# Kernel optimization log

Measured on AMD Instinct MI355X. Metric: run time of the kernel, lower is better.

## Reference

```python
import jax, jax.numpy as jnp
import numpy as np

BS, NA, NL, NF = 1024, 64, 32, 16   # batch, agents, num_link, num_link_fea
H, M, A = 32, 32, 16                # hidden_dim, message_dim, action_dim


def setup_inputs() -> dict:
    key = jax.random.key(0)
    ks = iter(jax.random.split(key, 64))
    def rn(shape, s=0.05):
        return jax.random.normal(next(ks), shape, jnp.float32) * s
    return {
        "states": jax.random.normal(next(ks), (BS, NA, NL, NF), jnp.float32),
        "hidden_state": jax.random.normal(next(ks), (BS, NA, H), jnp.float32),
        # input_attention (embed=32, heads=4)
        "ia_wq": rn((NF, H)), "ia_bq": jnp.zeros((H,), jnp.float32),
        "ia_wkv": rn((NF, 2 * H)), "ia_bkv": jnp.zeros((2 * H,), jnp.float32),
        "ia_wo": rn((H, NF)), "ia_bo": jnp.zeros((NF,), jnp.float32),
        "ln1_g": jnp.ones((NF,), jnp.float32), "ln1_b": jnp.zeros((NF,), jnp.float32),
        "il_w": rn((NL * NF, H)), "il_b": jnp.zeros((H,), jnp.float32),
        # GRUCell (gate order: r, z, n)
        "gru_wih": rn((H, 3 * H)), "gru_whh": rn((H, 3 * H)),
        "gru_bih": jnp.zeros((3 * H,), jnp.float32), "gru_bhh": jnp.zeros((3 * H,), jnp.float32),
        "ms_w": rn((H, H)), "ms_b": jnp.zeros((H,), jnp.float32),
        # per-agent message generators stacked [NA, H, M]
        "mg_w": rn((NA, H, M)), "mg_b": jnp.zeros((NA, M), jnp.float32),
        # attention_message (embed=32, heads=2)
        "ma_wq": rn((H, H)), "ma_bq": jnp.zeros((H,), jnp.float32),
        "ma_wkv": rn((M, 2 * H)), "ma_bkv": jnp.zeros((2 * H,), jnp.float32),
        "ma_wo": rn((H, H)), "ma_bo": jnp.zeros((H,), jnp.float32),
        "ln2_g": jnp.ones((H,), jnp.float32), "ln2_b": jnp.zeros((H,), jnp.float32),
        "qs_w": rn((H + M, H)), "qs_b": jnp.zeros((H,), jnp.float32),
        # per-agent Q heads stacked [NA, H, A]
        "ah_w": rn((NA, H, A)), "ah_b": jnp.zeros((NA, A), jnp.float32),
    }


def _ln(x, g, b, eps=1e-5):
    m = x.mean(-1, keepdims=True)
    v = ((x - m) ** 2).mean(-1, keepdims=True)
    return (x - m) * jax.lax.rsqrt(v + eps) * g + b


def _mha(q, kv, wq, bq, wkv, bkv, wo, bo, nh):
    # q, kv: [bs, na, sl, fd]
    bs, na, sl, _ = q.shape
    Q = q @ wq + bq
    K, V = jnp.split(kv @ wkv + bkv, 2, axis=-1)
    E = Q.shape[-1]
    hd = E // nh
    def sp(x):
        return x.reshape(bs, na, sl, nh, hd).transpose(0, 1, 3, 2, 4)  # [b,a,n,s,d]
    Qh, Kh, Vh = sp(Q), sp(K), sp(V)
    attn = jax.nn.softmax(
        jnp.einsum('banqd,bankd->banqk', Qh, Kh) * (1.0 / np.sqrt(hd)), axis=-1)
    o = jnp.einsum('banqk,bankd->banqd', attn, Vh)
    o = o.transpose(0, 1, 3, 2, 4).reshape(bs, na, sl, E)
    return o @ wo + bo


def reference(states, hidden_state,
              ia_wq, ia_bq, ia_wkv, ia_bkv, ia_wo, ia_bo,
              ln1_g, ln1_b, il_w, il_b,
              gru_wih, gru_whh, gru_bih, gru_bhh,
              ms_w, ms_b, mg_w, mg_b,
              ma_wq, ma_bq, ma_wkv, ma_bkv, ma_wo, ma_bo,
              ln2_g, ln2_b, qs_w, qs_b, ah_w, ah_b):
    bs, na, nl, nf = states.shape
    # self-attention over links + residual layernorm
    aft = _mha(states, states, ia_wq, ia_bq, ia_wkv, ia_bkv, ia_wo, ia_bo, 4)
    aft = _ln(states + aft, ln1_g, ln1_b)
    enc = aft.reshape(bs, na, nl * nf) @ il_w + il_b          # [bs, na, H]
    hprev = hidden_state.reshape(bs, na, -1)
    # GRUCell step (pytorch gate order r, z, n)
    gi = enc @ gru_wih + gru_bih
    gh = hprev @ gru_whh + gru_bhh
    ir, iz, ig = jnp.split(gi, 3, axis=-1)
    hr, hz, hg = jnp.split(gh, 3, axis=-1)
    r = jax.nn.sigmoid(ir + hr)
    z = jax.nn.sigmoid(iz + hz)
    n = jnp.tanh(ig + r * hg)
    h = (1.0 - z) * n + z * hprev                             # [bs, na, H]
    # per-agent messages
    memb = jax.nn.relu(h @ ms_w + ms_b)
    messages = jnp.einsum('bah,ahm->bam', memb, mg_w) + mg_b  # [bs, na, M]
    md = jax.lax.stop_gradient(messages)
    mean_message = (md.sum(1, keepdims=True) - md + messages) / na
    # communication attention (sl = 1) + residual layernorm
    after = _mha(h[:, :, None, :], mean_message[:, :, None, :],
                 ma_wq, ma_bq, ma_wkv, ma_bkv, ma_wo, ma_bo, 2)[:, :, 0, :]
    after = _ln(h + after, ln2_g, ln2_b)
    feat = jnp.concatenate([h, after], axis=-1)
    qemb = jax.nn.relu(feat @ qs_w + qs_b)
    q_values = jnp.einsum('bah,ahk->bak', qemb, ah_w) + ah_b  # [bs, na, A]
    return q_values, h, mean_message
```

## Files before the change

### kernel.cpp

```cpp
#include <hip/hip_runtime.h>

typedef unsigned int u32;
typedef _Float16 f16;
typedef f16 h2 __attribute__((ext_vector_type(2)));

#define QP     0
#define KVP    256
#define WOP    768
#define ILWP   1024
#define WIHP   9216
#define WHHP   11264
#define MSWP   13312
#define MGWP   13824
#define QSWP   46592
#define AHWP   47616
#define F32B   64000
#define BQ     (F32B+0)
#define BKV    (F32B+32)
#define BO     (F32B+96)
#define LN1G   (F32B+112)
#define LN1B   (F32B+128)
#define ILB    (F32B+144)
#define BIH    (F32B+176)
#define BHH    (F32B+272)
#define MSB    (F32B+368)
#define MGB    (F32B+400)
#define MAWKVV (F32B+2448)
#define MABKVV (F32B+3472)
#define MAWO   (F32B+3504)
#define MABO   (F32B+4528)
#define LN2G   (F32B+4560)
#define LN2B   (F32B+4592)
#define QSB    (F32B+4624)
#define AHB    (F32B+4656)
#define W_TOTAL (F32B+5680)
#define W_ALLOC 69696

#define OUT_Q  0
#define OUT_H  1048576
#define OUT_MM 3145728

#define CS (0.35355339059327373f * 1.4426950408889634f)

#if __has_builtin(__builtin_amdgcn_wave_barrier)
#define WB() __builtin_amdgcn_wave_barrier()
#else
#define WB() __threadfence_block()
#endif

#if __has_builtin(__builtin_amdgcn_exp2f)
__device__ __forceinline__ float EXP2(float x) { return __builtin_amdgcn_exp2f(x); }
#else
__device__ __forceinline__ float EXP2(float x) { return __expf(x * 0.6931471805599453f); }
#endif

#if __has_builtin(__builtin_amdgcn_fdot2)
__device__ __forceinline__ float FD(h2 a, h2 b, float c) {
    return __builtin_amdgcn_fdot2(a, b, c, false);
}
#else
__device__ __forceinline__ float FD(h2 a, h2 b, float c) {
    return c + (float)a.x * (float)b.x + (float)a.y * (float)b.y;
}
#endif

#if __has_builtin(__builtin_amdgcn_cvt_pkrtz)
__device__ __forceinline__ h2 pk2(float a, float b) {
    auto r = __builtin_amdgcn_cvt_pkrtz(a, b);
    h2 out;
    __builtin_memcpy(&out, &r, sizeof(out));
    return out;
}
#else
__device__ __forceinline__ h2 pk2(float a, float b) { h2 r; r.x = (f16)a; r.y = (f16)b; return r; }
#endif

__device__ __forceinline__ h2  u2h(u32 x) { union { u32 u; h2 h; } c; c.u = x; return c.h; }
__device__ __forceinline__ u32 h2u(h2 x)  { union { u32 u; h2 h; } c; c.h = x; return c.u; }

__device__ __forceinline__ float sigm(float x) { return 1.0f / (1.0f + __expf(-x)); }

struct WP { const float* p[30]; };

__global__ void kw_conv(WP wp, float* W) {
    u32* Wu = (u32*)W;
    int gid = blockIdx.x * blockDim.x + threadIdx.x;
    if (gid >= W_TOTAL) return;
    if (gid < KVP) {
        int e = gid >> 3, i = gid & 7;
        const float* wq = wp.p[0];
        Wu[gid] = h2u(pk2(wq[(2*i)*32 + e] * CS, wq[(2*i+1)*32 + e] * CS));
    } else if (gid < WOP) {
        int idx = gid - KVP; int e = idx >> 3, i = idx & 7;
        const float* wkv = wp.p[2];
        Wu[gid] = h2u(pk2(wkv[(2*i)*64 + e], wkv[(2*i+1)*64 + e]));
    } else if (gid < ILWP) {
        int idx = gid - WOP; int f = idx >> 4, i = idx & 15;
        const float* wo = wp.p[4];
        Wu[gid] = h2u(pk2(wo[(2*i)*16 + f], wo[(2*i+1)*16 + f]));
    } else if (gid < WIHP) {
        int idx = gid - ILWP;
        int jp4 = idx >> 7, t = (idx >> 2) & 31, i = idx & 3;
        int jp = jp4 * 4 + i;
        const float* ilw = wp.p[8];
        Wu[gid] = h2u(pk2(ilw[(2*jp)*32 + t], ilw[(2*jp+1)*32 + t]));
    } else if (gid < WHHP) {
        int idx = gid - WIHP;
        int kp = idx >> 7, t = (idx >> 2) & 31, j = idx & 3;
        const float* wih = wp.p[10];
        Wu[gid] = (j < 3) ? h2u(pk2(wih[(2*kp)*96 + j*32 + t], wih[(2*kp+1)*96 + j*32 + t])) : 0u;
    } else if (gid < MSWP) {
        int idx = gid - WHHP;
        int kp = idx >> 7, t = (idx >> 2) & 31, j = idx & 3;
        const float* whh = wp.p[11];
        Wu[gid] = (j < 3) ? h2u(pk2(whh[(2*kp)*96 + j*32 + t], whh[(2*kp+1)*96 + j*32 + t])) : 0u;
    } else if (gid < MGWP) {
        int idx = gid - MSWP; int kp = idx >> 5, t = idx & 31;
        const float* msw = wp.p[14];
        Wu[gid] = h2u(pk2(msw[(2*kp)*32 + t], msw[(2*kp+1)*32 + t]));
    } else if (gid < QSWP) {
        int idx = gid - MGWP; int a = idx >> 9, rem = idx & 511, kp = rem >> 5, m = rem & 31;
        const float* mgw = wp.p[16];
        Wu[gid] = h2u(pk2(mgw[(a*32 + 2*kp)*32 + m], mgw[(a*32 + 2*kp+1)*32 + m]));
    } else if (gid < AHWP) {
        int idx = gid - QSWP; int kp = idx >> 5, t = idx & 31;
        const float* qsw = wp.p[26];
        Wu[gid] = h2u(pk2(qsw[(2*kp)*32 + t], qsw[(2*kp+1)*32 + t]));
    } else if (gid < F32B) {
        int idx = gid - AHWP; int a = idx >> 8, rem = idx & 255, kp = rem >> 4, u = rem & 15;
        const float* ahw = wp.p[28];
        Wu[gid] = h2u(pk2(ahw[(a*32 + 2*kp)*16 + u], ahw[(a*32 + 2*kp+1)*16 + u]));
    } else {
        int i = gid - F32B;
        float v;
        if      (i < 32)   v = wp.p[1][i] * CS;
        else if (i < 96)   v = wp.p[3][i - 32];
        else if (i < 112)  v = wp.p[5][i - 96];
        else if (i < 128)  v = wp.p[6][i - 112];
        else if (i < 144)  v = wp.p[7][i - 128];
        else if (i < 176)  v = wp.p[9][i - 144];
        else if (i < 272)  v = wp.p[12][i - 176];
        else if (i < 368)  v = wp.p[13][i - 272];
        else if (i < 400)  v = wp.p[15][i - 368];
        else if (i < 2448) v = wp.p[17][i - 400];
        else if (i < 3472) { int j = i - 2448; v = wp.p[20][(j >> 5)*64 + 32 + (j & 31)]; }
        else if (i < 3504) v = wp.p[21][32 + (i - 3472)];
        else if (i < 4528) v = wp.p[22][i - 3504];
        else if (i < 4560) v = wp.p[23][i - 4528];
        else if (i < 4592) v = wp.p[24][i - 4560];
        else if (i < 4624) v = wp.p[25][i - 4592];
        else if (i < 4656) v = wp.p[27][i - 4624];
        else               v = wp.p[29][i - 4656];
        W[gid] = v;
    }
}

__global__ __launch_bounds__(256, 5) void k_main(
    const float* __restrict__ states, const float* __restrict__ hidden,
    const float* W, float* __restrict__ outp)
{
    const u32* Wu = (const u32*)W;

    __shared__ uint4 KbH[8][32][4];
    __shared__ uint4 VbH[8][32][4];

    const int w    = threadIdx.x >> 6;
    const int lane = threadIdx.x & 63;
    const int sub  = lane >> 5;
    const int t    = lane & 31;
    const int ag   = w * 2 + sub;
    const int pair = blockIdx.x * 4 + w;
    const int b    = pair >> 5;
    const int a    = ((pair & 31) << 1) | sub;
    const int ba   = b * 64 + a;

    float* scr = (float*)&VbH[ag][0][0];

    float s[16];
    {
        const float4* p4 = reinterpret_cast<const float4*>(states + ((size_t)ba * 32 + t) * 16);
        float4 f0 = p4[0], f1 = p4[1], f2 = p4[2], f3 = p4[3];
        s[0]=f0.x; s[1]=f0.y; s[2]=f0.z; s[3]=f0.w;
        s[4]=f1.x; s[5]=f1.y; s[6]=f1.z; s[7]=f1.w;
        s[8]=f2.x; s[9]=f2.y; s[10]=f2.z; s[11]=f2.w;
        s[12]=f3.x; s[13]=f3.y; s[14]=f3.z; s[15]=f3.w;
    }
    float hp = hidden[(size_t)ba * 32 + t];
    h2 sh[8];
    #pragma unroll
    for (int i = 0; i < 8; ++i) sh[i] = pk2(s[2*i], s[2*i+1]);

    h2 qh[16];
    #pragma unroll
    for (int j = 0; j < 16; ++j) {
        float a0 = W[BQ + 2*j], a1 = W[BQ + 2*j + 1];
        #pragma unroll
        for (int i = 0; i < 8; ++i) {
            a0 = FD(sh[i], u2h(Wu[QP + (2*j)*8 + i]), a0);
            a1 = FD(sh[i], u2h(Wu[QP + (2*j+1)*8 + i]), a1);
        }
        qh[j] = pk2(a0, a1);
    }
    #pragma unroll
    for (int u = 0; u < 4; ++u) {
        u32 kc[4], vc[4];
        #pragma unroll
        for (int c = 0; c < 4; ++c) {
            int e0 = u*8 + 2*c, e1 = e0 + 1;
            float k0 = W[BKV+e0], k1 = W[BKV+e1];
            float v0 = W[BKV+32+e0], v1 = W[BKV+32+e1];
            #pragma unroll
            for (int i = 0; i < 8; ++i) {
                k0 = FD(sh[i], u2h(Wu[KVP + e0*8 + i]), k0);
                k1 = FD(sh[i], u2h(Wu[KVP + e1*8 + i]), k1);
                v0 = FD(sh[i], u2h(Wu[KVP + (32+e0)*8 + i]), v0);
                v1 = FD(sh[i], u2h(Wu[KVP + (32+e1)*8 + i]), v1);
            }
            kc[c] = h2u(pk2(k0, k1)); vc[c] = h2u(pk2(v0, v1));
        }
        int uc = u ^ (t & 3);
        KbH[ag][t][uc] = make_uint4(kc[0], kc[1], kc[2], kc[3]);
        VbH[ag][t][uc] = make_uint4(vc[0], vc[1], vc[2], vc[3]);
    }
    WB();

    h2 oh[16];
    #pragma unroll
    for (int hh = 0; hh < 4; ++hh) {
        float l = 0.0f;
        h2 ov0 = {(f16)0, (f16)0}, ov1 = ov0, ov2 = ov0, ov3 = ov0;
        #pragma unroll
        for (int k = 0; k < 32; ++k) {
            uint4 kr = KbH[ag][k][hh ^ (k & 3)];
            float sc = 0.0f;
            sc = FD(qh[hh*4+0], u2h(kr.x), sc);
            sc = FD(qh[hh*4+1], u2h(kr.y), sc);
            sc = FD(qh[hh*4+2], u2h(kr.z), sc);
            sc = FD(qh[hh*4+3], u2h(kr.w), sc);
            float e = EXP2(sc);
            l += e;
            h2 ph = pk2(e, e);
            uint4 vr = VbH[ag][k][hh ^ (k & 3)];
            ov0 += ph * u2h(vr.x);
            ov1 += ph * u2h(vr.y);
            ov2 += ph * u2h(vr.z);
            ov3 += ph * u2h(vr.w);
        }
        float inv = 1.0f / l;
        h2 hinv = pk2(inv, inv);
        oh[hh*4+0] = ov0 * hinv; oh[hh*4+1] = ov1 * hinv;
        oh[hh*4+2] = ov2 * hinv; oh[hh*4+3] = ov3 * hinv;
    }
    WB();

    float aft[16];
    {
        float x[16];
        float mean = 0.0f;
        #pragma unroll
        for (int f = 0; f < 16; ++f) {
            float acc = W[BO + f];
            #pragma unroll
            for (int i = 0; i < 16; ++i) acc = FD(oh[i], u2h(Wu[WOP + f*16 + i]), acc);
            x[f] = s[f] + acc;
            mean += x[f];
        }
        mean *= (1.0f / 16.0f);
        float var = 0.0f;
        #pragma unroll
        for (int f = 0; f < 16; ++f) { float d = x[f] - mean; var += d * d; }
        var *= (1.0f / 16.0f);
        float rs = rsqrtf(var + 1e-5f);
        #pragma unroll
        for (int f = 0; f < 16; ++f)
            aft[f] = (x[f] - mean) * rs * W[LN1G + f] + W[LN1B + f];
    }
    uint4* aftA = &KbH[ag][0][0];
    {
        u32 ac[8];
        #pragma unroll
        for (int c = 0; c < 8; ++c) ac[c] = h2u(pk2(aft[2*c], aft[2*c+1]));
        aftA[2*t]     = make_uint4(ac[0], ac[1], ac[2], ac[3]);
        aftA[2*t + 1] = make_uint4(ac[4], ac[5], ac[6], ac[7]);
    }
    WB();

    float enc = W[ILB + t];
    {
        const uint4* aA   = aftA;
        const uint4* ilw4 = (const uint4*)(Wu + ILWP);
        #pragma unroll 8
        for (int jp4 = 0; jp4 < 64; ++jp4) {
            uint4 av = aA[jp4];
            uint4 wv = ilw4[jp4 * 32 + t];
            enc = FD(u2h(av.x), u2h(wv.x), enc);
            enc = FD(u2h(av.y), u2h(wv.y), enc);
            enc = FD(u2h(av.z), u2h(wv.z), enc);
            enc = FD(u2h(av.w), u2h(wv.w), enc);
        }
    }
    WB();
    scr[t] = enc;
    WB();

    float gi0 = W[BIH + t], gi1 = W[BIH + 32 + t], gi2 = W[BIH + 64 + t];
    float gh0 = W[BHH + t], gh1 = W[BHH + 32 + t], gh2 = W[BHH + 64 + t];
    {
        const float4* eF = (const float4*)scr;
        const float4* hF = (const float4*)(hidden + (size_t)ba * 32);
        const uint4* wi4 = (const uint4*)(Wu + WIHP);
        const uint4* wh4 = (const uint4*)(Wu + WHHP);
        #pragma unroll
        for (int q4 = 0; q4 < 8; ++q4) {
            float4 ev = eF[q4], hv = hF[q4];
            h2 ea = pk2(ev.x, ev.y), eb = pk2(ev.z, ev.w);
            h2 ha = pk2(hv.x, hv.y), hb = pk2(hv.z, hv.w);
            uint4 wiA = wi4[(q4*2)*32 + t], wiB = wi4[(q4*2+1)*32 + t];
            uint4 whA = wh4[(q4*2)*32 + t], whB = wh4[(q4*2+1)*32 + t];
            gi0 = FD(ea, u2h(wiA.x), gi0); gi1 = FD(ea, u2h(wiA.y), gi1); gi2 = FD(ea, u2h(wiA.z), gi2);
            gi0 = FD(eb, u2h(wiB.x), gi0); gi1 = FD(eb, u2h(wiB.y), gi1); gi2 = FD(eb, u2h(wiB.z), gi2);
            gh0 = FD(ha, u2h(whA.x), gh0); gh1 = FD(ha, u2h(whA.y), gh1); gh2 = FD(ha, u2h(whA.z), gh2);
            gh0 = FD(hb, u2h(whB.x), gh0); gh1 = FD(hb, u2h(whB.y), gh1); gh2 = FD(hb, u2h(whB.z), gh2);
        }
    }
    float r  = sigm(gi0 + gh0);
    float z  = sigm(gi1 + gh1);
    float n  = tanhf(gi2 + r * gh2);
    float hn = (1.0f - z) * n + z * hp;
    outp[OUT_H + (size_t)ba * 32 + t] = hn;
    WB();
    scr[64 + t] = hn;
    WB();

    {
        const float4* nF = (const float4*)(scr + 64);
        float mb = W[MSB + t];
        #pragma unroll
        for (int q4 = 0; q4 < 8; ++q4) {
            float4 v = nF[q4];
            h2 a2 = pk2(v.x, v.y), b2 = pk2(v.z, v.w);
            mb = FD(a2, u2h(Wu[MSWP + (q4*2)*32 + t]), mb);
            mb = FD(b2, u2h(Wu[MSWP + (q4*2+1)*32 + t]), mb);
        }
        mb = fmaxf(mb, 0.0f);
        WB();
        scr[96 + t] = mb;
        WB();
    }
    {
        const float4* mF = (const float4*)(scr + 96);
        float mg = W[MGB + a * 32 + t];
        #pragma unroll
        for (int q4 = 0; q4 < 8; ++q4) {
            float4 v = mF[q4];
            h2 a2 = pk2(v.x, v.y), b2 = pk2(v.z, v.w);
            mg = FD(a2, u2h(Wu[MGWP + a*512 + (q4*2)*32 + t]), mg);
            mg = FD(b2, u2h(Wu[MGWP + a*512 + (q4*2+1)*32 + t]), mg);
        }
        outp[OUT_MM + (size_t)ba * 32 + t] = mg;
    }
}

__global__ __launch_bounds__(512) void k_mean(const float* W, float* __restrict__ ao_ws,
                                              float* __restrict__ outp)
{
    const int b   = blockIdx.x;
    const int tid = threadIdx.x;
    const int t   = tid & 31;
    const int c   = tid >> 5;
    __shared__ float pS[16][32];
    __shared__ float mmS[32];

    float acc = 0.0f;
    #pragma unroll
    for (int a2 = 0; a2 < 4; ++a2)
        acc += outp[OUT_MM + ((size_t)b * 64 + (a2 * 16 + c)) * 32 + t];
    pS[c][t] = acc;
    __syncthreads();
    if (tid < 32) {
        float ssum = 0.0f;
        #pragma unroll
        for (int cc = 0; cc < 16; ++cc) ssum += pS[cc][t];
        mmS[t] = ssum * (1.0f / 64.0f);
    }
    __syncthreads();
    {
        float mv = mmS[t];
        #pragma unroll
        for (int i = 0; i < 4; ++i)
            outp[OUT_MM + (size_t)b * 2048 + i * 512 + tid] = mv;
    }
    if (tid < 32) {
        float v = W[MABKVV + t];
        #pragma unroll 8
        for (int k = 0; k < 32; ++k) v += mmS[k] * W[MAWKVV + k * 32 + t];
        float o = W[MABO + t];
        #pragma unroll 8
        for (int k = 0; k < 32; ++k) o += __shfl(v, k, 64) * W[MAWO + k * 32 + t];
        ao_ws[b * 32 + t] = o;
    }
}

__global__ __launch_bounds__(512) void k_tail(
    const float* __restrict__ ao_ws, const float* W, float* __restrict__ outp)
{
    const u32* Wu = (const u32*)W;
    __shared__ __align__(16) float featS[16][64];
    __shared__ __align__(16) float qeS[16][32];
    const int w    = threadIdx.x >> 6;
    const int lane = threadIdx.x & 63;
    const int sub  = lane >> 5;
    const int t    = lane & 31;
    const int ag   = w * 2 + sub;
    const int pair = blockIdx.x * 8 + w;
    const int b    = pair >> 5;
    const int a    = ((pair & 31) << 1) | sub;
    const int ba   = b * 64 + a;

    float h  = outp[OUT_H + (size_t)ba * 32 + t];
    float ao = ao_ws[b * 32 + t];
    float x  = h + ao;
    float sm = x;
    #pragma unroll
    for (int m2 = 1; m2 < 32; m2 <<= 1) sm += __shfl_xor(sm, m2, 64);
    float mean = sm * (1.0f / 32.0f);
    float dx = x - mean;
    float vv = dx * dx;
    #pragma unroll
    for (int m2 = 1; m2 < 32; m2 <<= 1) vv += __shfl_xor(vv, m2, 64);
    float var   = vv * (1.0f / 32.0f);
    float after = dx * rsqrtf(var + 1e-5f) * W[LN2G + t] + W[LN2B + t];

    featS[ag][t]      = h;
    featS[ag][32 + t] = after;
    WB();
    {
        const float4* fF = (const float4*)&featS[ag][0];
        float acc = W[QSB + t];
        #pragma unroll
        for (int q4 = 0; q4 < 16; ++q4) {
            float4 v = fF[q4];
            h2 a2 = pk2(v.x, v.y), b2 = pk2(v.z, v.w);
            acc = FD(a2, u2h(Wu[QSWP + (q4*2)*32 + t]), acc);
            acc = FD(b2, u2h(Wu[QSWP + (q4*2+1)*32 + t]), acc);
        }
        acc = fmaxf(acc, 0.0f);
        WB();
        qeS[ag][t] = acc;
        WB();
    }
    if (t < 16) {
        const float4* qF = (const float4*)&qeS[ag][0];
        float qa = W[AHB + a * 16 + t];
        #pragma unroll
        for (int q4 = 0; q4 < 8; ++q4) {
            float4 v = qF[q4];
            h2 a2 = pk2(v.x, v.y), b2 = pk2(v.z, v.w);
            qa = FD(a2, u2h(Wu[AHWP + a*256 + (q4*2)*16 + t]), qa);
            qa = FD(b2, u2h(Wu[AHWP + a*256 + (q4*2+1)*16 + t]), qa);
        }
        outp[OUT_Q + (size_t)ba * 16 + t] = qa;
    }
}

extern "C" void kernel_launch(void* const* d_in, const int* in_sizes, int n_in,
                              void* d_out, int out_size, void* d_ws, size_t ws_size,
                              hipStream_t stream) {
    (void)in_sizes; (void)n_in; (void)out_size; (void)ws_size;
    WP wp;
    for (int i = 0; i < 30; ++i) wp.p[i] = (const float*)d_in[i + 2];

    float* W     = (float*)d_ws;
    float* ao_ws = W + W_ALLOC;

    const float* states = (const float*)d_in[0];
    const float* hidden = (const float*)d_in[1];
    float* outp = (float*)d_out;

    kw_conv<<<dim3((W_TOTAL + 255) / 256), dim3(256), 0, stream>>>(wp, W);
    k_main<<<dim3(8192), dim3(256), 0, stream>>>(states, hidden, W, outp);
    k_mean<<<dim3(1024), dim3(512), 0, stream>>>(W, ao_ws, outp);
    k_tail<<<dim3(4096), dim3(512), 0, stream>>>(ao_ws, W, outp);
}
```

Baseline: 446.0 us.

## Compute input attention with 32x32x16 MFMA instead of per-lane dot products

The per-link input attention (Q/K/V projections, QK^T scores, softmax, PV and output projection) in k_main is moved from per-thread fdot2 loops and shared-memory K/V buffers onto MFMA 32x32x16 f16 instructions. Each wave now handles one agent at a time across all 64 lanes, looping over its two agents. New pre-transposed weight layouts are produced by the conversion kernel to match the MFMA operand layout. The goal is to cut the VALU-heavy attention cost, at the price of more registers (launch bounds lowered from 5 to 4) and extra weight-prep work.

```diff
diff --git a/kernel.cpp b/kernel.cpp
--- a/kernel.cpp
+++ b/kernel.cpp
@@ -3,6 +3,8 @@
 typedef unsigned int u32;
 typedef _Float16 f16;
 typedef f16 h2 __attribute__((ext_vector_type(2)));
+typedef __attribute__((ext_vector_type(8)))  _Float16 f16x8;
+typedef __attribute__((ext_vector_type(16))) float    f32x16;
 
 #define QP     0
 #define KVP    256
@@ -34,13 +36,21 @@
 #define QSB    (F32B+4624)
 #define AHB    (F32B+4656)
 #define W_TOTAL (F32B+5680)
-#define W_ALLOC 69696
+#define QTA    69680
+#define KTA    69936
+#define WVB    70192
+#define WOTA   70448
+#define BQT    70960
+#define BKT    70992
+#define BOT    71024
+#define W_TOTAL2 71056
+#define W_ALLOC  71104
 
 #define OUT_Q  0
 #define OUT_H  1048576
 #define OUT_MM 3145728
 
-#define CS (0.35355339059327373f * 1.4426950408889634f)
+#define CS2 (0.5f * 0.35355339059327373f * 1.4426950408889634f)
 
 #if __has_builtin(__builtin_amdgcn_wave_barrier)
 #define WB() __builtin_amdgcn_wave_barrier()
@@ -77,6 +87,10 @@
 
 __device__ __forceinline__ h2  u2h(u32 x) { union { u32 u; h2 h; } c; c.u = x; return c.h; }
 __device__ __forceinline__ u32 h2u(h2 x)  { union { u32 u; h2 h; } c; c.h = x; return c.u; }
+__device__ __forceinline__ f16x8 mk8(u32 a, u32 b, u32 c, u32 d) {
+    union { u32 u[4]; f16x8 v; } x; x.u[0]=a; x.u[1]=b; x.u[2]=c; x.u[3]=d; return x.v;
+}
+#define MFMA32(a,b,c) __builtin_amdgcn_mfma_f32_32x32x16_f16(a, b, c, 0, 0, 0)
 
 __device__ __forceinline__ float sigm(float x) { return 1.0f / (1.0f + __expf(-x)); }
 
@@ -85,11 +99,11 @@
 __global__ void kw_conv(WP wp, float* W) {
     u32* Wu = (u32*)W;
     int gid = blockIdx.x * blockDim.x + threadIdx.x;
-    if (gid >= W_TOTAL) return;
+    if (gid >= W_TOTAL2) return;
     if (gid < KVP) {
         int e = gid >> 3, i = gid & 7;
         const float* wq = wp.p[0];
-        Wu[gid] = h2u(pk2(wq[(2*i)*32 + e] * CS, wq[(2*i+1)*32 + e] * CS));
+        Wu[gid] = h2u(pk2(wq[(2*i)*32 + e], wq[(2*i+1)*32 + e]));
     } else if (gid < WOP) {
         int idx = gid - KVP; int e = idx >> 3, i = idx & 7;
         const float* wkv = wp.p[2];
@@ -130,10 +144,10 @@
         int idx = gid - AHWP; int a = idx >> 8, rem = idx & 255, kp = rem >> 4, u = rem & 15;
         const float* ahw = wp.p[28];
         Wu[gid] = h2u(pk2(ahw[(a*32 + 2*kp)*16 + u], ahw[(a*32 + 2*kp+1)*16 + u]));
-    } else {
+    } else if (gid < W_TOTAL) {
         int i = gid - F32B;
         float v;
-        if      (i < 32)   v = wp.p[1][i] * CS;
+        if      (i < 32)   v = wp.p[1][i];
         else if (i < 96)   v = wp.p[3][i - 32];
         else if (i < 112)  v = wp.p[5][i - 96];
         else if (i < 128)  v = wp.p[6][i - 112];
@@ -152,142 +166,178 @@
         else if (i < 4656) v = wp.p[27][i - 4624];
         else               v = wp.p[29][i - 4656];
         W[gid] = v;
-    }
-}
-
-__global__ __launch_bounds__(256, 5) void k_main(
+    } else if (gid < KTA) {
+        int idx = gid - QTA; int l = idx >> 2, j = idx & 3;
+        int g = l & 31, hf = l >> 5;
+        int k0 = (j < 2) ? (4*hf + 2*j) : (8 + 4*hf + 2*(j-2));
+        const float* wq = wp.p[0];
+        Wu[gid] = h2u(pk2(wq[k0*32 + g] * CS2, wq[(k0+1)*32 + g] * CS2));
+    } else if (gid < WVB) {
+        int idx = gid - KTA; int l = idx >> 2, j = idx & 3;
+        int g = l & 31, hf = l >> 5;
+        int k0 = (j < 2) ? (4*hf + 2*j) : (8 + 4*hf + 2*(j-2));
+        const float* wkv = wp.p[2];
+        Wu[gid] = h2u(pk2(wkv[k0*64 + g], wkv[(k0+1)*64 + g]));
+    } else if (gid < WOTA) {
+        int idx = gid - WVB; int l = idx >> 2, j = idx & 3;
+        int n = l & 31, hf = l >> 5;
+        int k0 = (j < 2) ? (4*hf + 2*j) : (8 + 4*hf + 2*(j-2));
+        const float* wkv = wp.p[2];
+        Wu[gid] = h2u(pk2(wkv[k0*64 + 32 + n], wkv[(k0+1)*64 + 32 + n]));
+    } else if (gid < BQT) {
+        int idx = gid - WOTA; int kh = idx >> 8, rem = idx & 255;
+        int l = rem >> 2, j = rem & 3;
+        int g = l & 31, hf = l >> 5;
+        int f0 = kh*16 + ((j < 2) ? (4*hf + 2*j) : (8 + 4*hf + 2*(j-2)));
+        const float* wo = wp.p[4];
+        Wu[gid] = (g < 16) ? h2u(pk2(wo[f0*16 + g], wo[(f0+1)*16 + g])) : 0u;
+    } else {
+        int i = gid - BQT;
+        int hf = (i >> 4) & 1, r = i & 15;
+        int row = (r & 3) + 8*(r >> 2) + 4*hf;
+        float v;
+        if      (i < 32) v = wp.p[1][row] * CS2;
+        else if (i < 64) v = wp.p[3][row];
+        else             v = (row < 16) ? wp.p[5][row] : 0.0f;
+        W[gid] = v;
+    }
+}
+
+__global__ __launch_bounds__(256, 4) void k_main(
     const float* __restrict__ states, const float* __restrict__ hidden,
     const float* W, float* __restrict__ outp)
 {
     const u32* Wu = (const u32*)W;
 
-    __shared__ uint4 KbH[8][32][4];
-    __shared__ uint4 VbH[8][32][4];
+    __shared__ __align__(16) u32   aftL[8][256];
+    __shared__ __align__(16) float encS[8][32];
+    __shared__ __align__(16) float hnS[8][32];
+    __shared__ __align__(16) float membS[8][32];
 
     const int w    = threadIdx.x >> 6;
     const int lane = threadIdx.x & 63;
     const int sub  = lane >> 5;
     const int t    = lane & 31;
-    const int ag   = w * 2 + sub;
+    const int hf   = sub;
     const int pair = blockIdx.x * 4 + w;
     const int b    = pair >> 5;
     const int a    = ((pair & 31) << 1) | sub;
     const int ba   = b * 64 + a;
 
-    float* scr = (float*)&VbH[ag][0][0];
-
-    float s[16];
-    {
-        const float4* p4 = reinterpret_cast<const float4*>(states + ((size_t)ba * 32 + t) * 16);
-        float4 f0 = p4[0], f1 = p4[1], f2 = p4[2], f3 = p4[3];
-        s[0]=f0.x; s[1]=f0.y; s[2]=f0.z; s[3]=f0.w;
-        s[4]=f1.x; s[5]=f1.y; s[6]=f1.z; s[7]=f1.w;
-        s[8]=f2.x; s[9]=f2.y; s[10]=f2.z; s[11]=f2.w;
-        s[12]=f3.x; s[13]=f3.y; s[14]=f3.z; s[15]=f3.w;
-    }
     float hp = hidden[(size_t)ba * 32 + t];
-    h2 sh[8];
-    #pragma unroll
-    for (int i = 0; i < 8; ++i) sh[i] = pk2(s[2*i], s[2*i+1]);
-
-    h2 qh[16];
-    #pragma unroll
-    for (int j = 0; j < 16; ++j) {
-        float a0 = W[BQ + 2*j], a1 = W[BQ + 2*j + 1];
-        #pragma unroll
-        for (int i = 0; i < 8; ++i) {
-            a0 = FD(sh[i], u2h(Wu[QP + (2*j)*8 + i]), a0);
-            a1 = FD(sh[i], u2h(Wu[QP + (2*j+1)*8 + i]), a1);
-        }
-        qh[j] = pk2(a0, a1);
-    }
-    #pragma unroll
-    for (int u = 0; u < 4; ++u) {
-        u32 kc[4], vc[4];
-        #pragma unroll
-        for (int c = 0; c < 4; ++c) {
-            int e0 = u*8 + 2*c, e1 = e0 + 1;
-            float k0 = W[BKV+e0], k1 = W[BKV+e1];
-            float v0 = W[BKV+32+e0], v1 = W[BKV+32+e1];
+
+    f16x8 wqa = mk8(Wu[QTA + lane*4+0], Wu[QTA + lane*4+1], Wu[QTA + lane*4+2], Wu[QTA + lane*4+3]);
+    f16x8 wka = mk8(Wu[KTA + lane*4+0], Wu[KTA + lane*4+1], Wu[KTA + lane*4+2], Wu[KTA + lane*4+3]);
+    f16x8 wvb = mk8(Wu[WVB + lane*4+0], Wu[WVB + lane*4+1], Wu[WVB + lane*4+2], Wu[WVB + lane*4+3]);
+    float bv  = W[BKV + 32 + t];
+
+    for (int ap = 0; ap < 2; ++ap) {
+        const int ag2 = w * 2 + ap;
+        const int baA = b * 64 + (((pair & 31) << 1) | ap);
+        const float* sp = states + (size_t)baA * 512;
+        float4 f0 = *reinterpret_cast<const float4*>(sp + t*16 + 4*hf);
+        float4 f1 = *reinterpret_cast<const float4*>(sp + t*16 + 8 + 4*hf);
+        float sv[8] = {f0.x,f0.y,f0.z,f0.w, f1.x,f1.y,f1.z,f1.w};
+        f16x8 sf = mk8(h2u(pk2(f0.x,f0.y)), h2u(pk2(f0.z,f0.w)),
+                       h2u(pk2(f1.x,f1.y)), h2u(pk2(f1.z,f1.w)));
+
+        f32x16 cc;
+        #pragma unroll
+        for (int r = 0; r < 16; ++r) cc[r] = W[BQT + hf*16 + r];
+        f32x16 dq = MFMA32(wqa, sf, cc);
+        #pragma unroll
+        for (int r = 0; r < 16; ++r) cc[r] = W[BKT + hf*16 + r];
+        f32x16 dk = MFMA32(wka, sf, cc);
+        #pragma unroll
+        for (int r = 0; r < 16; ++r) cc[r] = bv;
+        f32x16 dv = MFMA32(sf, wvb, cc);
+
+        u32 qp[8], kp[8];
+        #pragma unroll
+        for (int h = 0; h < 4; ++h) {
+            qp[2*h]   = h2u(pk2(dq[4*h],   dq[4*h+1]));
+            qp[2*h+1] = h2u(pk2(dq[4*h+2], dq[4*h+3]));
+            kp[2*h]   = h2u(pk2(dk[4*h],   dk[4*h+1]));
+            kp[2*h+1] = h2u(pk2(dk[4*h+2], dk[4*h+3]));
+        }
+        f16x8 vaf = mk8(h2u(pk2(dv[0],dv[1])),  h2u(pk2(dv[2],dv[3])),
+                        h2u(pk2(dv[4],dv[5])),  h2u(pk2(dv[6],dv[7])));
+        f16x8 vbf = mk8(h2u(pk2(dv[8],dv[9])),  h2u(pk2(dv[10],dv[11])),
+                        h2u(pk2(dv[12],dv[13])),h2u(pk2(dv[14],dv[15])));
+
+        f32x16 zro;
+        #pragma unroll
+        for (int r = 0; r < 16; ++r) zro[r] = 0.0f;
+
+        u32 oa[4], ob[4];
+        #pragma unroll
+        for (int h = 0; h < 4; ++h) {
+            f16x8 ak = mk8(kp[2*h], kp[2*h+1], kp[2*h], kp[2*h+1]);
+            f16x8 bq = mk8(qp[2*h], qp[2*h+1], qp[2*h], qp[2*h+1]);
+            f32x16 ds = MFMA32(ak, bq, zro);
+            f32x16 p;
+            float ls = 0.0f;
             #pragma unroll
-            for (int i = 0; i < 8; ++i) {
-                k0 = FD(sh[i], u2h(Wu[KVP + e0*8 + i]), k0);
-                k1 = FD(sh[i], u2h(Wu[KVP + e1*8 + i]), k1);
-                v0 = FD(sh[i], u2h(Wu[KVP + (32+e0)*8 + i]), v0);
-                v1 = FD(sh[i], u2h(Wu[KVP + (32+e1)*8 + i]), v1);
+            for (int r = 0; r < 16; ++r) { p[r] = EXP2(ds[r]); ls += p[r]; }
+            ls += __shfl_xor(ls, 32, 64);
+            float inv = 1.0f / ls;
+            f16x8 paf = mk8(h2u(pk2(p[0]*inv, p[1]*inv)),  h2u(pk2(p[2]*inv, p[3]*inv)),
+                            h2u(pk2(p[4]*inv, p[5]*inv)),  h2u(pk2(p[6]*inv, p[7]*inv)));
+            f16x8 pbf = mk8(h2u(pk2(p[8]*inv, p[9]*inv)),  h2u(pk2(p[10]*inv,p[11]*inv)),
+                            h2u(pk2(p[12]*inv,p[13]*inv)), h2u(pk2(p[14]*inv,p[15]*inv)));
+            f32x16 dt = MFMA32(vaf, paf, zro);
+            dt = MFMA32(vbf, pbf, dt);
+            if (h < 2) {
+                oa[2*h]   = h2u(pk2(dt[4*h],   dt[4*h+1]));
+                oa[2*h+1] = h2u(pk2(dt[4*h+2], dt[4*h+3]));
+            } else {
+                ob[2*(h-2)]   = h2u(pk2(dt[4*h],   dt[4*h+1]));
+                ob[2*(h-2)+1] = h2u(pk2(dt[4*h+2], dt[4*h+3]));
             }
-            kc[c] = h2u(pk2(k0, k1)); vc[c] = h2u(pk2(v0, v1));
-        }
-        int uc = u ^ (t & 3);
-        KbH[ag][t][uc] = make_uint4(kc[0], kc[1], kc[2], kc[3]);
-        VbH[ag][t][uc] = make_uint4(vc[0], vc[1], vc[2], vc[3]);
+        }
+        f16x8 wo0 = mk8(Wu[WOTA + lane*4+0], Wu[WOTA + lane*4+1],
+                        Wu[WOTA + lane*4+2], Wu[WOTA + lane*4+3]);
+        f16x8 wo1 = mk8(Wu[WOTA + 256 + lane*4+0], Wu[WOTA + 256 + lane*4+1],
+                        Wu[WOTA + 256 + lane*4+2], Wu[WOTA + 256 + lane*4+3]);
+        f32x16 ca;
+        #pragma unroll
+        for (int r = 0; r < 16; ++r) ca[r] = W[BOT + hf*16 + r];
+        f32x16 da = MFMA32(wo0, mk8(oa[0],oa[1],oa[2],oa[3]), ca);
+        da = MFMA32(wo1, mk8(ob[0],ob[1],ob[2],ob[3]), da);
+
+        float x[8];
+        float sm = 0.0f;
+        #pragma unroll
+        for (int r = 0; r < 8; ++r) { x[r] = da[r] + sv[r]; sm += x[r]; }
+        sm += __shfl_xor(sm, 32, 64);
+        float mean = sm * (1.0f / 16.0f);
+        float vv = 0.0f;
+        #pragma unroll
+        for (int r = 0; r < 8; ++r) { float d = x[r] - mean; vv += d * d; }
+        vv += __shfl_xor(vv, 32, 64);
+        float rs = rsqrtf(vv * (1.0f / 16.0f) + 1e-5f);
+        float4 g0 = *reinterpret_cast<const float4*>(W + LN1G + 4*hf);
+        float4 g1 = *reinterpret_cast<const float4*>(W + LN1G + 8 + 4*hf);
+        float4 e0 = *reinterpret_cast<const float4*>(W + LN1B + 4*hf);
+        float4 e1 = *reinterpret_cast<const float4*>(W + LN1B + 8 + 4*hf);
+        float gam[8] = {g0.x,g0.y,g0.z,g0.w, g1.x,g1.y,g1.z,g1.w};
+        float bet[8] = {e0.x,e0.y,e0.z,e0.w, e1.x,e1.y,e1.z,e1.w};
+        float af[8];
+        #pragma unroll
+        for (int r = 0; r < 8; ++r) af[r] = (x[r] - mean) * rs * gam[r] + bet[r];
+        int i0 = t * 8 + 2 * hf;
+        aftL[ag2][i0]     = h2u(pk2(af[0], af[1]));
+        aftL[ag2][i0 + 1] = h2u(pk2(af[2], af[3]));
+        aftL[ag2][i0 + 4] = h2u(pk2(af[4], af[5]));
+        aftL[ag2][i0 + 5] = h2u(pk2(af[6], af[7]));
     }
     WB();
 
-    h2 oh[16];
-    #pragma unroll
-    for (int hh = 0; hh < 4; ++hh) {
-        float l = 0.0f;
-        h2 ov0 = {(f16)0, (f16)0}, ov1 = ov0, ov2 = ov0, ov3 = ov0;
-        #pragma unroll
-        for (int k = 0; k < 32; ++k) {
-            uint4 kr = KbH[ag][k][hh ^ (k & 3)];
-            float sc = 0.0f;
-            sc = FD(qh[hh*4+0], u2h(kr.x), sc);
-            sc = FD(qh[hh*4+1], u2h(kr.y), sc);
-            sc = FD(qh[hh*4+2], u2h(kr.z), sc);
-            sc = FD(qh[hh*4+3], u2h(kr.w), sc);
-            float e = EXP2(sc);
-            l += e;
-            h2 ph = pk2(e, e);
-            uint4 vr = VbH[ag][k][hh ^ (k & 3)];
-            ov0 += ph * u2h(vr.x);
-            ov1 += ph * u2h(vr.y);
-            ov2 += ph * u2h(vr.z);
-            ov3 += ph * u2h(vr.w);
-        }
-        float inv = 1.0f / l;
-        h2 hinv = pk2(inv, inv);
-        oh[hh*4+0] = ov0 * hinv; oh[hh*4+1] = ov1 * hinv;
-        oh[hh*4+2] = ov2 * hinv; oh[hh*4+3] = ov3 * hinv;
-    }
-    WB();
-
-    float aft[16];
-    {
-        float x[16];
-        float mean = 0.0f;
-        #pragma unroll
-        for (int f = 0; f < 16; ++f) {
-            float acc = W[BO + f];
-            #pragma unroll
-            for (int i = 0; i < 16; ++i) acc = FD(oh[i], u2h(Wu[WOP + f*16 + i]), acc);
-            x[f] = s[f] + acc;
-            mean += x[f];
-        }
-        mean *= (1.0f / 16.0f);
-        float var = 0.0f;
-        #pragma unroll
-        for (int f = 0; f < 16; ++f) { float d = x[f] - mean; var += d * d; }
-        var *= (1.0f / 16.0f);
-        float rs = rsqrtf(var + 1e-5f);
-        #pragma unroll
-        for (int f = 0; f < 16; ++f)
-            aft[f] = (x[f] - mean) * rs * W[LN1G + f] + W[LN1B + f];
-    }
-    uint4* aftA = &KbH[ag][0][0];
-    {
-        u32 ac[8];
-        #pragma unroll
-        for (int c = 0; c < 8; ++c) ac[c] = h2u(pk2(aft[2*c], aft[2*c+1]));
-        aftA[2*t]     = make_uint4(ac[0], ac[1], ac[2], ac[3]);
-        aftA[2*t + 1] = make_uint4(ac[4], ac[5], ac[6], ac[7]);
-    }
-    WB();
+    const int ag = w * 2 + sub;
 
     float enc = W[ILB + t];
     {
-        const uint4* aA   = aftA;
+        const uint4* aA   = (const uint4*)&aftL[ag][0];
         const uint4* ilw4 = (const uint4*)(Wu + ILWP);
         #pragma unroll 8
         for (int jp4 = 0; jp4 < 64; ++jp4) {
@@ -300,13 +350,13 @@
         }
     }
     WB();
-    scr[t] = enc;
+    encS[ag][t] = enc;
     WB();
 
     float gi0 = W[BIH + t], gi1 = W[BIH + 32 + t], gi2 = W[BIH + 64 + t];
     float gh0 = W[BHH + t], gh1 = W[BHH + 32 + t], gh2 = W[BHH + 64 + t];
     {
-        const float4* eF = (const float4*)scr;
+        const float4* eF = (const float4*)&encS[ag][0];
         const float4* hF = (const float4*)(hidden + (size_t)ba * 32);
         const uint4* wi4 = (const uint4*)(Wu + WIHP);
         const uint4* wh4 = (const uint4*)(Wu + WHHP);
@@ -329,11 +379,11 @@
     float hn = (1.0f - z) * n + z * hp;
     outp[OUT_H + (size_t)ba * 32 + t] = hn;
     WB();
-    scr[64 + t] = hn;
+    hnS[ag][t] = hn;
     WB();
 
     {
-        const float4* nF = (const float4*)(scr + 64);
+        const float4* nF = (const float4*)&hnS[ag][0];
         float mb = W[MSB + t];
         #pragma unroll
         for (int q4 = 0; q4 < 8; ++q4) {
@@ -344,11 +394,11 @@
         }
         mb = fmaxf(mb, 0.0f);
         WB();
-        scr[96 + t] = mb;
+        membS[ag][t] = mb;
         WB();
     }
     {
-        const float4* mF = (const float4*)(scr + 96);
+        const float4* mF = (const float4*)&membS[ag][0];
         float mg = W[MGB + a * 32 + t];
         #pragma unroll
         for (int q4 = 0; q4 < 8; ++q4) {
@@ -477,7 +527,7 @@
     const float* hidden = (const float*)d_in[1];
     float* outp = (float*)d_out;
 
-    kw_conv<<<dim3((W_TOTAL + 255) / 256), dim3(256), 0, stream>>>(wp, W);
+    kw_conv<<<dim3((W_TOTAL2 + 255) / 256), dim3(256), 0, stream>>>(wp, W);
     k_main<<<dim3(8192), dim3(256), 0, stream>>>(states, hidden, W, outp);
     k_mean<<<dim3(1024), dim3(512), 0, stream>>>(W, ao_ws, outp);
     k_tail<<<dim3(4096), dim3(512), 0, stream>>>(ao_ws, W, outp);
```

Measured after the change: 558.8 us. 25.3% more time.
